# Kernel tuning notes

Measured on AMD Instinct MI355X. Metric: run time of the kernel, lower is better.

Reference implementation:

```python
import jax, jax.numpy as jnp
import numpy as np

B, T, DM = 4, 1024, 1024
H, NW = 16, 16
HD = DM // H  # 64


def _l2norm(x, eps=1e-12):
    n = jnp.sqrt(jnp.sum(x * x, axis=-1, keepdims=True))
    return x / jnp.maximum(n, eps)


def setup_inputs() -> dict:
    key = jax.random.key(0)
    ks = jax.random.split(key, 14)
    s = 0.02
    d = {
        "x": jax.random.normal(ks[0], (B, T, DM), jnp.float32),
        "Wqf": jax.random.normal(ks[1], (H * NW, DM), jnp.float32) * s,
        "bqf": jnp.zeros((H * NW,), jnp.float32),
        "Wkf": jax.random.normal(ks[2], (H * NW, DM), jnp.float32) * s,
        "bkf": jnp.zeros((H * NW,), jnp.float32),
        "Wqp": jax.random.normal(ks[3], (H * NW, DM), jnp.float32) * s,
        "bqp": jnp.zeros((H * NW,), jnp.float32),
        "Wkp": jax.random.normal(ks[4], (H * NW, DM), jnp.float32) * s,
        "bkp": jnp.zeros((H * NW,), jnp.float32),
        "Wv": jax.random.normal(ks[5], (DM, DM), jnp.float32) * s,
        "bv": jnp.zeros((DM,), jnp.float32),
        "Wo": jax.random.normal(ks[6], (DM, DM), jnp.float32) * s,
        "bo": jnp.zeros((DM,), jnp.float32),
        "inter_scale": jnp.ones((H, 1, 1), jnp.float32),
    }
    return d


def reference(x, Wqf, bqf, Wkf, bkf, Wqp, bqp, Wkp, bkp, Wv, bv, Wo, bo, inter_scale):
    b, t, c = x.shape
    # projections -> [b, H, t, NW]
    def proj(W, bb, w_last):
        return (x @ W.T + bb).reshape(b, t, H, w_last).transpose(0, 2, 1, 3)

    q_f = proj(Wqf, bqf, NW)
    k_f = proj(Wkf, bkf, NW)
    q_p = proj(Wqp, bqp, NW)
    k_p = proj(Wkp, bkp, NW)
    v = proj(Wv, bv, HD)  # [b,H,t,HD]

    t_pos = jnp.arange(t, dtype=x.dtype)[None, None, :, None]  # [1,1,t,1]
    q_waves = jnp.sin(q_f * t_pos + q_p)
    k_waves = jnp.sin(k_f * t_pos + k_p)

    scale_factor = NW ** 0.25
    q_norm = _l2norm(q_waves) * scale_factor
    k_norm = _l2norm(k_waves) * scale_factor

    # wave interference scores [b,H,t,t]
    interference = jnp.einsum('bhtw,bhsw->bhts', q_norm, k_norm)
    interference = interference * inter_scale  # broadcast [H,1,1]

    causal = jnp.tril(jnp.ones((t, t), dtype=bool))  # True = attended
    # elu_plus_one kernel; masked positions -> elu(-inf)+1 == 0
    attn = jnp.where(causal, jax.nn.elu(interference) + 1.0, 0.0)

    num_attended = jnp.arange(1, t + 1, dtype=x.dtype)[None, None, :, None]
    attn = attn / jnp.sqrt(num_attended)

    out = jnp.einsum('bhts,bhsd->bhtd', attn, v)  # [b,H,t,HD]
    out = out.transpose(0, 2, 1, 3).reshape(b, t, c)
    return out @ Wo.T + bo
```

## Files before the change

kernel.cpp:

```cpp
#include <hip/hip_runtime.h>
#include <math.h>

typedef __attribute__((ext_vector_type(8))) short bf16x8;
typedef __attribute__((ext_vector_type(4))) float f32x4;
typedef __attribute__((ext_vector_type(4))) int i32x4;

typedef __attribute__((address_space(3))) void lds_void;
typedef __attribute__((address_space(1))) const void glb_cvoid;

__device__ __forceinline__ unsigned short f32_to_bf16(float f) {
    unsigned u = __float_as_uint(f);
    unsigned r = (u + 0x7FFFu + ((u >> 16) & 1u)) >> 16;
    return (unsigned short)r;
}
__device__ __forceinline__ float bf16_to_f32(unsigned short h) {
    return __uint_as_float(((unsigned)h) << 16);
}

__global__ __launch_bounds__(256)
void split_bf16(const float* __restrict__ src, unsigned short* __restrict__ hi,
                unsigned short* __restrict__ lo, int n4)
{
    const int i = blockIdx.x * 256 + threadIdx.x;
    if (i >= n4) return;
    float4 v = *reinterpret_cast<const float4*>(src + (size_t)i * 4);
    ushort4 h;
    h.x = f32_to_bf16(v.x); h.y = f32_to_bf16(v.y);
    h.z = f32_to_bf16(v.z); h.w = f32_to_bf16(v.w);
    *reinterpret_cast<ushort4*>(hi + (size_t)i * 4) = h;
    if (lo) {
        ushort4 l;
        l.x = f32_to_bf16(v.x - bf16_to_f32(h.x));
        l.y = f32_to_bf16(v.y - bf16_to_f32(h.y));
        l.z = f32_to_bf16(v.z - bf16_to_f32(h.z));
        l.w = f32_to_bf16(v.w - bf16_to_f32(h.w));
        *reinterpret_cast<ushort4*>(lo + (size_t)i * 4) = l;
    }
}

__global__ __launch_bounds__(256)
void split4_bf16(const float* __restrict__ W0, const float* __restrict__ W1,
                 const float* __restrict__ W2, const float* __restrict__ W3,
                 unsigned short* __restrict__ hi, unsigned short* __restrict__ lo)
{
    const int i = blockIdx.x * 256 + threadIdx.x;
    const int sel = i >> 16, j = i & 65535;
    const float* W = (sel == 0) ? W0 : (sel == 1) ? W1 : (sel == 2) ? W2 : W3;
    float4 v = *reinterpret_cast<const float4*>(W + (size_t)j * 4);
    ushort4 h, l;
    h.x = f32_to_bf16(v.x); h.y = f32_to_bf16(v.y);
    h.z = f32_to_bf16(v.z); h.w = f32_to_bf16(v.w);
    l.x = f32_to_bf16(v.x - bf16_to_f32(h.x));
    l.y = f32_to_bf16(v.y - bf16_to_f32(h.y));
    l.z = f32_to_bf16(v.z - bf16_to_f32(h.z));
    l.w = f32_to_bf16(v.w - bf16_to_f32(h.w));
    const size_t o = (size_t)sel * 262144 + (size_t)j * 4;
    *reinterpret_cast<ushort4*>(hi + o) = h;
    *reinterpret_cast<ushort4*>(lo + o) = l;
}

template <int MODE>
__global__ __launch_bounds__(256)
void mfma_gemm(const unsigned short* __restrict__ A0,
               const unsigned short* __restrict__ A1,
               const unsigned short* __restrict__ B0,
               const unsigned short* __restrict__ B1,
               const float* __restrict__ bias,
               float* __restrict__ outF, unsigned short* __restrict__ outH)
{
    __shared__ __attribute__((aligned(16))) unsigned short Al[128 * 64];
    __shared__ __attribute__((aligned(16))) unsigned short Bl[64 * 64];

    const int tid = threadIdx.x;
    const int w = tid >> 6, l = tid & 63;
    const int bm = blockIdx.y * 128, bn = blockIdx.x * 64;
    const int KTOT = (MODE == 0) ? 3072 : 1024;
    const int wr = w >> 1, wc = w & 1;
    const int lr = l & 15, lg = l >> 4;
    const int r8 = l >> 3;
    const int c8 = l & 7;
    const int csw = (c8 ^ r8) << 3;

    f32x4 acc[4][2];
#pragma unroll
    for (int i = 0; i < 4; i++)
#pragma unroll
        for (int j = 0; j < 2; j++)
#pragma unroll
            for (int r = 0; r < 4; r++) acc[i][j][r] = 0.f;

    for (int k0 = 0; k0 < KTOT; k0 += 64) {
        const unsigned short* Aseg = A0;
        const unsigned short* Bseg = B0;
        int kc = k0;
        if (MODE == 0) {
            const int seg = k0 >> 10;
            kc = k0 & 1023;
            if (seg == 1) Aseg = A1;
            if (seg == 2) Bseg = B1;
        }
#pragma unroll
        for (int i = 0; i < 4; i++) {
            const int ar = w * 32 + i * 8 + r8;
            __builtin_amdgcn_global_load_lds(
                (glb_cvoid*)(Aseg + (size_t)(bm + ar) * 1024 + kc + csw),
                (lds_void*)(&Al[(w * 32 + i * 8) * 64]), 16, 0, 0);
        }
#pragma unroll
        for (int i = 0; i < 2; i++) {
            const int br = w * 16 + i * 8 + r8;
            __builtin_amdgcn_global_load_lds(
                (glb_cvoid*)(Bseg + (size_t)(bn + br) * 1024 + kc + csw),
                (lds_void*)(&Bl[(w * 16 + i * 8) * 64]), 16, 0, 0);
        }
        __syncthreads();

        bf16x8 af[4][2], bfr[2][2];
#pragma unroll
        for (int i = 0; i < 4; i++)
#pragma unroll
            for (int kk = 0; kk < 2; kk++)
                af[i][kk] = *reinterpret_cast<const bf16x8*>(
                    &Al[(wr * 64 + i * 16 + lr) * 64 +
                        (((kk * 4 + lg) ^ (lr & 7)) << 3)]);
#pragma unroll
        for (int j = 0; j < 2; j++)
#pragma unroll
            for (int kk = 0; kk < 2; kk++)
                bfr[j][kk] = *reinterpret_cast<const bf16x8*>(
                    &Bl[(wc * 32 + j * 16 + lr) * 64 +
                        (((kk * 4 + lg) ^ (lr & 7)) << 3)]);
#pragma unroll
        for (int kk = 0; kk < 2; kk++)
#pragma unroll
            for (int i = 0; i < 4; i++)
#pragma unroll
                for (int j = 0; j < 2; j++)
                    acc[i][j] = __builtin_amdgcn_mfma_f32_16x16x32_bf16(
                        af[i][kk], bfr[j][kk], acc[i][j], 0, 0, 0);
        __syncthreads();
    }

#pragma unroll
    for (int i = 0; i < 4; i++) {
#pragma unroll
        for (int j = 0; j < 2; j++) {
#pragma unroll
            for (int r = 0; r < 4; r++) {
                const int row = bm + wr * 64 + i * 16 + lg * 4 + r;
                const int col = bn + wc * 32 + j * 16 + lr;
                float v = acc[i][j][r];
                if (MODE == 0) {
                    outF[(size_t)row * 1024 + col] = v;
                } else if (MODE == 1) {
                    v += bias[col];
                    const int hh = col >> 6, d = col & 63;
                    const int b = row >> 10, t = row & 1023;
                    outH[(((size_t)(b * 16 + hh) * 64 + d) * 1024) + t] =
                        f32_to_bf16(v);
                } else {
                    outF[(size_t)row * 1024 + col] = v + bias[col];
                }
            }
        }
    }
}

__global__ __launch_bounds__(256)
void wave_norm(const float* __restrict__ raw,
               const float* __restrict__ bqf, const float* __restrict__ bkf,
               const float* __restrict__ bqp, const float* __restrict__ bkp,
               unsigned short* __restrict__ qn, unsigned short* __restrict__ kn)
{
    const int row = blockIdx.x;
    const int b = row >> 10, t = row & 1023;
    const int tid = threadIdx.x;
    const float tf = (float)t;

    const float qf = raw[(size_t)row * 1024 + tid]        + bqf[tid];
    const float kf = raw[(size_t)row * 1024 + 256 + tid]  + bkf[tid];
    const float qp = raw[(size_t)row * 1024 + 512 + tid]  + bqp[tid];
    const float kp = raw[(size_t)row * 1024 + 768 + tid]  + bkp[tid];

    const float sq = sinf(fmaf(qf, tf, qp));
    const float sk = sinf(fmaf(kf, tf, kp));

    float nq = sq * sq, nk = sk * sk;
#pragma unroll
    for (int off = 8; off >= 1; off >>= 1) {
        nq += __shfl_xor(nq, off, 16);
        nk += __shfl_xor(nk, off, 16);
    }
    const float qv = sq * 2.0f / fmaxf(sqrtf(nq), 1e-12f);
    const float kv = sk * 2.0f / fmaxf(sqrtf(nk), 1e-12f);

    const int h = tid >> 4, ww = tid & 15;
    const size_t o = ((size_t)(b * 16 + h) * 1024 + t) * 16 + ww;
    qn[o] = f32_to_bf16(qv);
    kn[o] = f32_to_bf16(kv);
}

__global__ __launch_bounds__(512)
void wave_attn_mfma(const unsigned short* __restrict__ qn,
                    const unsigned short* __restrict__ kn,
                    const unsigned short* __restrict__ vtt,
                    const float* __restrict__ iscale,
                    unsigned short* __restrict__ y)
{
    const int p = blockIdx.x, bh = blockIdx.y;
    const int h = bh & 15, b = bh >> 4;
    const int tid = threadIdx.x;
    const int wq = tid >> 6;
    const int l = tid & 63;
    const int lt = l & 15;
    const int gl = l >> 4;
    const int it = (wq < 4) ? p : (15 - p);
    const int t0w = it * 64 + (wq & 3) * 16;
    const float scale = iscale[h];
    const int tmine = t0w + lt;

    const bf16x8 zero8 = {0, 0, 0, 0, 0, 0, 0, 0};
    const f32x4 zf = {0.f, 0.f, 0.f, 0.f};
    const size_t kb = (size_t)bh * 1024;

    bf16x8 bq = zero8;
    if (gl < 2)
        bq = *reinterpret_cast<const bf16x8*>(&qn[(kb + t0w + lt) * 16 + gl * 8]);

    f32x4 o[4];
#pragma unroll
    for (int jd = 0; jd < 4; jd++) o[jd] = zf;

    const int addr0 = ((2 * (gl & 1)) * 16 + lt) * 4;
    const int addr1 = addr0 + 64;
    const bool hi = ((gl >> 1) & 1) != 0;

    bf16x8 akc[4], akn[4];
#pragma unroll
    for (int js = 0; js < 4; js++) {
        akc[js] = zero8;
        if (gl < 2)
            akc[js] = *reinterpret_cast<const bf16x8*>(
                &kn[(kb + js * 16 + lt) * 16 + gl * 8]);
    }

    for (int is = 0; is <= it; is++) {
        const int s0 = is * 64;

        if (is < it) {
#pragma unroll
            for (int js = 0; js < 4; js++) {
                akn[js] = zero8;
                if (gl < 2)
                    akn[js] = *reinterpret_cast<const bf16x8*>(
                        &kn[(kb + s0 + 64 + js * 16 + lt) * 16 + gl * 8]);
            }
        }
        bf16x8 bv[2][4];
#pragma unroll
        for (int ks = 0; ks < 2; ks++)
#pragma unroll
            for (int jd = 0; jd < 4; jd++)
                bv[ks][jd] = *reinterpret_cast<const bf16x8*>(
                    &vtt[((size_t)(bh * 64 + jd * 16 + lt)) * 1024 +
                         s0 + ks * 32 + gl * 8]);

        f32x4 st[4];
#pragma unroll
        for (int js = 0; js < 4; js++)
            st[js] = __builtin_amdgcn_mfma_f32_16x16x32_bf16(
                akc[js], bq, zf, 0, 0, 0);

        int pk[4][2];
#pragma unroll
        for (int js = 0; js < 4; js++) {
            float pp[4];
#pragma unroll
            for (int r = 0; r < 4; r++) {
                const int s = s0 + js * 16 + gl * 4 + r;
                const float xv = st[js][r] * scale;
                const float phi = (xv > 0.f) ? (xv + 1.0f) : __expf(xv);
                pp[r] = (s <= tmine) ? phi : 0.f;
            }
            asm("v_cvt_pk_bf16_f32 %0, %1, %2"
                : "=v"(pk[js][0]) : "v"(pp[0]), "v"(pp[1]));
            asm("v_cvt_pk_bf16_f32 %0, %1, %2"
                : "=v"(pk[js][1]) : "v"(pp[2]), "v"(pp[3]));
        }

        int rg[4][2][2];
#pragma unroll
        for (int js = 0; js < 4; js++)
#pragma unroll
            for (int sl = 0; sl < 2; sl++) {
                rg[js][sl][0] = __builtin_amdgcn_ds_bpermute(addr0, pk[js][sl]);
                rg[js][sl][1] = __builtin_amdgcn_ds_bpermute(addr1, pk[js][sl]);
            }

#pragma unroll
        for (int ks = 0; ks < 2; ks++) {
            i32x4 au;
#pragma unroll
            for (int c = 0; c < 2; c++)
#pragma unroll
                for (int sl = 0; sl < 2; sl++)
                    au[2 * c + sl] = hi ? rg[2 * ks + 1][sl][c]
                                        : rg[2 * ks][sl][c];
            const bf16x8 pa = __builtin_bit_cast(bf16x8, au);
#pragma unroll
            for (int jd = 0; jd < 4; jd++)
                o[jd] = __builtin_amdgcn_mfma_f32_16x16x32_bf16(
                    pa, bv[ks][jd], o[jd], 0, 0, 0);
        }

#pragma unroll
        for (int js = 0; js < 4; js++) akc[js] = akn[js];
    }

#pragma unroll
    for (int r = 0; r < 4; r++) {
        const int t = t0w + gl * 4 + r;
        const float inv = rsqrtf((float)(t + 1));
#pragma unroll
        for (int jd = 0; jd < 4; jd++) {
            const int d = jd * 16 + lt;
            y[((size_t)b * 1024 + t) * 1024 + h * 64 + d] =
                f32_to_bf16(o[jd][r] * inv);
        }
    }
}

extern "C" void kernel_launch(void* const* d_in, const int* in_sizes, int n_in,
                              void* d_out, int out_size, void* d_ws, size_t ws_size,
                              hipStream_t stream)
{
    const float* x   = (const float*)d_in[0];
    const float* Wqf = (const float*)d_in[1];
    const float* bqf = (const float*)d_in[2];
    const float* Wkf = (const float*)d_in[3];
    const float* bkf = (const float*)d_in[4];
    const float* Wqp = (const float*)d_in[5];
    const float* bqp = (const float*)d_in[6];
    const float* Wkp = (const float*)d_in[7];
    const float* bkp = (const float*)d_in[8];
    const float* Wv  = (const float*)d_in[9];
    const float* bv  = (const float*)d_in[10];
    const float* Wo  = (const float*)d_in[11];
    const float* bo  = (const float*)d_in[12];
    const float* isc = (const float*)d_in[13];
    float* out = (float*)d_out;

    char* ws = (char*)d_ws;
    float*          raw = (float*)(ws);
    unsigned short* ybf = (unsigned short*)(ws);
    unsigned short* xh  = (unsigned short*)(ws + (16u << 20));
    unsigned short* xl  = (unsigned short*)(ws + (24u << 20));
    unsigned short* vtt = (unsigned short*)(ws + (24u << 20));
    unsigned short* WfH = (unsigned short*)(ws + (32u << 20));
    unsigned short* WfL = (unsigned short*)(ws + (34u << 20));
    unsigned short* qn  = (unsigned short*)(ws + (34u << 20));
    unsigned short* kn  = (unsigned short*)(ws + (36u << 20));
    unsigned short* WvH = WfH;
    unsigned short* WoH = WfH;

    split_bf16<<<4096, 256, 0, stream>>>(x, xh, xl, 1048576);
    split4_bf16<<<1024, 256, 0, stream>>>(Wqf, Wkf, Wqp, Wkp, WfH, WfL);

    mfma_gemm<0><<<dim3(16, 32), 256, 0, stream>>>(
        xh, xl, WfH, WfL, nullptr, raw, nullptr);

    split_bf16<<<1024, 256, 0, stream>>>(Wv, WvH, nullptr, 262144);
    mfma_gemm<1><<<dim3(16, 32), 256, 0, stream>>>(
        xh, nullptr, WvH, nullptr, bv, nullptr, vtt);

    wave_norm<<<4096, 256, 0, stream>>>(raw, bqf, bkf, bqp, bkp, qn, kn);

    wave_attn_mfma<<<dim3(8, 64), 512, 0, stream>>>(qn, kn, vtt, isc, ybf);

    split_bf16<<<1024, 256, 0, stream>>>(Wo, WoH, nullptr, 262144);
    mfma_gemm<2><<<dim3(16, 32), 256, 0, stream>>>(
        ybf, nullptr, WoH, nullptr, bo, out, nullptr);
}
```

Baseline: 227.9 us.

## Fuse freq/phase projection GEMM with sine wave normalization epilogue

Replaces the separate 4096x1024 fp32 projection GEMM plus wave_norm pass with one kernel. It computes the frequency GEMM (3-pass bf16 split precision) and the phase GEMM (hi-only bf16) into separate accumulators over the same tile, then applies sin, L2 norm and the bf16 store in the epilogue. This removes the 16MB fp32 raw intermediate write and read and one kernel launch, and drops the lo-split on the phase weights. It also adds an XCD-aware tile remap to all GEMMs. Phase precision drops to single bf16, and the fused GEMM uses smaller 64x64 tiles.

```diff
diff --git a/kernel.cpp b/kernel.cpp
--- a/kernel.cpp
+++ b/kernel.cpp
@@ -39,48 +39,173 @@
 }
 
 __global__ __launch_bounds__(256)
-void split4_bf16(const float* __restrict__ W0, const float* __restrict__ W1,
-                 const float* __restrict__ W2, const float* __restrict__ W3,
-                 unsigned short* __restrict__ hi, unsigned short* __restrict__ lo)
+void split4_bf16(const float* __restrict__ Wqf, const float* __restrict__ Wkf,
+                 const float* __restrict__ Wqp, const float* __restrict__ Wkp,
+                 unsigned short* __restrict__ WfH, unsigned short* __restrict__ WfL,
+                 unsigned short* __restrict__ WpH)
 {
     const int i = blockIdx.x * 256 + threadIdx.x;
     const int sel = i >> 16, j = i & 65535;
-    const float* W = (sel == 0) ? W0 : (sel == 1) ? W1 : (sel == 2) ? W2 : W3;
+    const float* W = (sel == 0) ? Wqf : (sel == 1) ? Wkf : (sel == 2) ? Wqp : Wkp;
     float4 v = *reinterpret_cast<const float4*>(W + (size_t)j * 4);
-    ushort4 h, l;
+    ushort4 h;
     h.x = f32_to_bf16(v.x); h.y = f32_to_bf16(v.y);
     h.z = f32_to_bf16(v.z); h.w = f32_to_bf16(v.w);
-    l.x = f32_to_bf16(v.x - bf16_to_f32(h.x));
-    l.y = f32_to_bf16(v.y - bf16_to_f32(h.y));
-    l.z = f32_to_bf16(v.z - bf16_to_f32(h.z));
-    l.w = f32_to_bf16(v.w - bf16_to_f32(h.w));
-    const size_t o = (size_t)sel * 262144 + (size_t)j * 4;
-    *reinterpret_cast<ushort4*>(hi + o) = h;
-    *reinterpret_cast<ushort4*>(lo + o) = l;
-}
-
-template <int MODE>
+    const size_t o = (size_t)(sel & 1) * 262144 + (size_t)j * 4;
+    if (sel < 2) {
+        *reinterpret_cast<ushort4*>(WfH + o) = h;
+        ushort4 l;
+        l.x = f32_to_bf16(v.x - bf16_to_f32(h.x));
+        l.y = f32_to_bf16(v.y - bf16_to_f32(h.y));
+        l.z = f32_to_bf16(v.z - bf16_to_f32(h.z));
+        l.w = f32_to_bf16(v.w - bf16_to_f32(h.w));
+        *reinterpret_cast<ushort4*>(WfL + o) = l;
+    } else {
+        *reinterpret_cast<ushort4*>(WpH + o) = h;
+    }
+}
+
+__device__ __forceinline__ void xcd_tiles(int& tm, int& tn) {
+    const int L = blockIdx.x + gridDim.x * blockIdx.y;
+    const int nbn = gridDim.x;
+    const int q3 = L >> 3;
+    tn = q3 % nbn;
+    tm = (L & 7) + 8 * (q3 / nbn);
+}
+
 __global__ __launch_bounds__(256)
-void mfma_gemm(const unsigned short* __restrict__ A0,
-               const unsigned short* __restrict__ A1,
-               const unsigned short* __restrict__ B0,
-               const unsigned short* __restrict__ B1,
-               const float* __restrict__ bias,
-               float* __restrict__ outF, unsigned short* __restrict__ outH)
-{
-    __shared__ __attribute__((aligned(16))) unsigned short Al[128 * 64];
+void freq_gemm_norm(const unsigned short* __restrict__ xh,
+                    const unsigned short* __restrict__ xl,
+                    const unsigned short* __restrict__ WfH,
+                    const unsigned short* __restrict__ WfL,
+                    const unsigned short* __restrict__ WpH,
+                    const float* __restrict__ bqf, const float* __restrict__ bkf,
+                    const float* __restrict__ bqp, const float* __restrict__ bkp,
+                    unsigned short* __restrict__ qn, unsigned short* __restrict__ kn)
+{
+    __shared__ __attribute__((aligned(16))) unsigned short Al[64 * 64];
     __shared__ __attribute__((aligned(16))) unsigned short Bl[64 * 64];
+
+    int tm, tn;
+    xcd_tiles(tm, tn);
+    const int bm = tm * 64, bn = tn * 64;
 
     const int tid = threadIdx.x;
     const int w = tid >> 6, l = tid & 63;
-    const int bm = blockIdx.y * 128, bn = blockIdx.x * 64;
-    const int KTOT = (MODE == 0) ? 3072 : 1024;
     const int wr = w >> 1, wc = w & 1;
     const int lr = l & 15, lg = l >> 4;
     const int r8 = l >> 3;
     const int c8 = l & 7;
     const int csw = (c8 ^ r8) << 3;
 
+    f32x4 accF[2][2], accP[2][2];
+#pragma unroll
+    for (int i = 0; i < 2; i++)
+#pragma unroll
+        for (int j = 0; j < 2; j++)
+#pragma unroll
+            for (int r = 0; r < 4; r++) { accF[i][j][r] = 0.f; accP[i][j][r] = 0.f; }
+
+    for (int k0 = 0; k0 < 4096; k0 += 64) {
+        const int seg = k0 >> 10;
+        const int kc = k0 & 1023;
+        const unsigned short* Aseg = (seg == 1) ? xl : xh;
+        const unsigned short* Bseg = (seg <= 1) ? WfH : (seg == 2) ? WfL : WpH;
+
+#pragma unroll
+        for (int i = 0; i < 2; i++) {
+            __builtin_amdgcn_global_load_lds(
+                (glb_cvoid*)(Aseg + (size_t)(bm + w * 16 + i * 8 + r8) * 1024 + kc + csw),
+                (lds_void*)(&Al[(w * 16 + i * 8) * 64]), 16, 0, 0);
+            __builtin_amdgcn_global_load_lds(
+                (glb_cvoid*)(Bseg + (size_t)(bn + w * 16 + i * 8 + r8) * 1024 + kc + csw),
+                (lds_void*)(&Bl[(w * 16 + i * 8) * 64]), 16, 0, 0);
+        }
+        __syncthreads();
+
+        bf16x8 af[2][2], bfr[2][2];
+#pragma unroll
+        for (int i = 0; i < 2; i++)
+#pragma unroll
+            for (int kk = 0; kk < 2; kk++) {
+                af[i][kk] = *reinterpret_cast<const bf16x8*>(
+                    &Al[(wr * 32 + i * 16 + lr) * 64 + (((kk * 4 + lg) ^ (lr & 7)) << 3)]);
+                bfr[i][kk] = *reinterpret_cast<const bf16x8*>(
+                    &Bl[(wc * 32 + i * 16 + lr) * 64 + (((kk * 4 + lg) ^ (lr & 7)) << 3)]);
+            }
+        if (seg < 3) {
+#pragma unroll
+            for (int kk = 0; kk < 2; kk++)
+#pragma unroll
+                for (int i = 0; i < 2; i++)
+#pragma unroll
+                    for (int j = 0; j < 2; j++)
+                        accF[i][j] = __builtin_amdgcn_mfma_f32_16x16x32_bf16(
+                            af[i][kk], bfr[j][kk], accF[i][j], 0, 0, 0);
+        } else {
+#pragma unroll
+            for (int kk = 0; kk < 2; kk++)
+#pragma unroll
+                for (int i = 0; i < 2; i++)
+#pragma unroll
+                    for (int j = 0; j < 2; j++)
+                        accP[i][j] = __builtin_amdgcn_mfma_f32_16x16x32_bf16(
+                            af[i][kk], bfr[j][kk], accP[i][j], 0, 0, 0);
+        }
+        __syncthreads();
+    }
+
+#pragma unroll
+    for (int i = 0; i < 2; i++) {
+#pragma unroll
+        for (int j = 0; j < 2; j++) {
+            const int col = bn + wc * 32 + j * 16 + lr;
+            const bool isQ = col < 256;
+            const int c = col & 255;
+            const float bf = isQ ? bqf[c] : bkf[c];
+            const float bp = isQ ? bqp[c] : bkp[c];
+            unsigned short* dst = isQ ? qn : kn;
+            const int h = c >> 4, ww = c & 15;
+#pragma unroll
+            for (int r = 0; r < 4; r++) {
+                const int row = bm + wr * 32 + i * 16 + lg * 4 + r;
+                const int b = row >> 10, t = row & 1023;
+                const float f = accF[i][j][r] + bf;
+                const float p = accP[i][j][r] + bp;
+                const float s = sinf(fmaf(f, (float)t, p));
+                float n2 = s * s;
+#pragma unroll
+                for (int off = 8; off >= 1; off >>= 1)
+                    n2 += __shfl_xor(n2, off);
+                const float val = s * 2.0f / fmaxf(sqrtf(n2), 1e-12f);
+                dst[((size_t)(b * 16 + h) * 1024 + t) * 16 + ww] = f32_to_bf16(val);
+            }
+        }
+    }
+}
+
+template <int MODE>
+__global__ __launch_bounds__(256)
+void mfma_gemm(const unsigned short* __restrict__ A0,
+               const unsigned short* __restrict__ B0,
+               const float* __restrict__ bias,
+               float* __restrict__ outF, unsigned short* __restrict__ outH)
+{
+    __shared__ __attribute__((aligned(16))) unsigned short Al[128 * 64];
+    __shared__ __attribute__((aligned(16))) unsigned short Bl[64 * 64];
+
+    int tm, tn;
+    xcd_tiles(tm, tn);
+    const int bm = tm * 128, bn = tn * 64;
+
+    const int tid = threadIdx.x;
+    const int w = tid >> 6, l = tid & 63;
+    const int wr = w >> 1, wc = w & 1;
+    const int lr = l & 15, lg = l >> 4;
+    const int r8 = l >> 3;
+    const int c8 = l & 7;
+    const int csw = (c8 ^ r8) << 3;
+
     f32x4 acc[4][2];
 #pragma unroll
     for (int i = 0; i < 4; i++)
@@ -89,28 +214,17 @@
 #pragma unroll
             for (int r = 0; r < 4; r++) acc[i][j][r] = 0.f;
 
-    for (int k0 = 0; k0 < KTOT; k0 += 64) {
-        const unsigned short* Aseg = A0;
-        const unsigned short* Bseg = B0;
-        int kc = k0;
-        if (MODE == 0) {
-            const int seg = k0 >> 10;
-            kc = k0 & 1023;
-            if (seg == 1) Aseg = A1;
-            if (seg == 2) Bseg = B1;
-        }
+    for (int k0 = 0; k0 < 1024; k0 += 64) {
 #pragma unroll
         for (int i = 0; i < 4; i++) {
-            const int ar = w * 32 + i * 8 + r8;
             __builtin_amdgcn_global_load_lds(
-                (glb_cvoid*)(Aseg + (size_t)(bm + ar) * 1024 + kc + csw),
+                (glb_cvoid*)(A0 + (size_t)(bm + w * 32 + i * 8 + r8) * 1024 + k0 + csw),
                 (lds_void*)(&Al[(w * 32 + i * 8) * 64]), 16, 0, 0);
         }
 #pragma unroll
         for (int i = 0; i < 2; i++) {
-            const int br = w * 16 + i * 8 + r8;
             __builtin_amdgcn_global_load_lds(
-                (glb_cvoid*)(Bseg + (size_t)(bn + br) * 1024 + kc + csw),
+                (glb_cvoid*)(B0 + (size_t)(bn + w * 16 + i * 8 + r8) * 1024 + k0 + csw),
                 (lds_void*)(&Bl[(w * 16 + i * 8) * 64]), 16, 0, 0);
         }
         __syncthreads();
@@ -121,15 +235,13 @@
 #pragma unroll
             for (int kk = 0; kk < 2; kk++)
                 af[i][kk] = *reinterpret_cast<const bf16x8*>(
-                    &Al[(wr * 64 + i * 16 + lr) * 64 +
-                        (((kk * 4 + lg) ^ (lr & 7)) << 3)]);
+                    &Al[(wr * 64 + i * 16 + lr) * 64 + (((kk * 4 + lg) ^ (lr & 7)) << 3)]);
 #pragma unroll
         for (int j = 0; j < 2; j++)
 #pragma unroll
             for (int kk = 0; kk < 2; kk++)
                 bfr[j][kk] = *reinterpret_cast<const bf16x8*>(
-                    &Bl[(wc * 32 + j * 16 + lr) * 64 +
-                        (((kk * 4 + lg) ^ (lr & 7)) << 3)]);
+                    &Bl[(wc * 32 + j * 16 + lr) * 64 + (((kk * 4 + lg) ^ (lr & 7)) << 3)]);
 #pragma unroll
         for (int kk = 0; kk < 2; kk++)
 #pragma unroll
@@ -149,55 +261,18 @@
             for (int r = 0; r < 4; r++) {
                 const int row = bm + wr * 64 + i * 16 + lg * 4 + r;
                 const int col = bn + wc * 32 + j * 16 + lr;
-                float v = acc[i][j][r];
-                if (MODE == 0) {
-                    outF[(size_t)row * 1024 + col] = v;
-                } else if (MODE == 1) {
-                    v += bias[col];
+                float v = acc[i][j][r] + bias[col];
+                if (MODE == 1) {
                     const int hh = col >> 6, d = col & 63;
                     const int b = row >> 10, t = row & 1023;
                     outH[(((size_t)(b * 16 + hh) * 64 + d) * 1024) + t] =
                         f32_to_bf16(v);
                 } else {
-                    outF[(size_t)row * 1024 + col] = v + bias[col];
+                    outF[(size_t)row * 1024 + col] = v;
                 }
             }
         }
     }
-}
-
-__global__ __launch_bounds__(256)
-void wave_norm(const float* __restrict__ raw,
-               const float* __restrict__ bqf, const float* __restrict__ bkf,
-               const float* __restrict__ bqp, const float* __restrict__ bkp,
-               unsigned short* __restrict__ qn, unsigned short* __restrict__ kn)
-{
-    const int row = blockIdx.x;
-    const int b = row >> 10, t = row & 1023;
-    const int tid = threadIdx.x;
-    const float tf = (float)t;
-
-    const float qf = raw[(size_t)row * 1024 + tid]        + bqf[tid];
-    const float kf = raw[(size_t)row * 1024 + 256 + tid]  + bkf[tid];
-    const float qp = raw[(size_t)row * 1024 + 512 + tid]  + bqp[tid];
-    const float kp = raw[(size_t)row * 1024 + 768 + tid]  + bkp[tid];
-
-    const float sq = sinf(fmaf(qf, tf, qp));
-    const float sk = sinf(fmaf(kf, tf, kp));
-
-    float nq = sq * sq, nk = sk * sk;
-#pragma unroll
-    for (int off = 8; off >= 1; off >>= 1) {
-        nq += __shfl_xor(nq, off, 16);
-        nk += __shfl_xor(nk, off, 16);
-    }
-    const float qv = sq * 2.0f / fmaxf(sqrtf(nq), 1e-12f);
-    const float kv = sk * 2.0f / fmaxf(sqrtf(nk), 1e-12f);
-
-    const int h = tid >> 4, ww = tid & 15;
-    const size_t o = ((size_t)(b * 16 + h) * 1024 + t) * 16 + ww;
-    qn[o] = f32_to_bf16(qv);
-    kn[o] = f32_to_bf16(kv);
 }
 
 __global__ __launch_bounds__(512)
@@ -351,33 +426,29 @@
     float* out = (float*)d_out;
 
     char* ws = (char*)d_ws;
-    float*          raw = (float*)(ws);
     unsigned short* ybf = (unsigned short*)(ws);
+    unsigned short* qn  = (unsigned short*)(ws + ( 8u << 20));
+    unsigned short* kn  = (unsigned short*)(ws + (10u << 20));
+    unsigned short* WfH = (unsigned short*)(ws + (12u << 20));
+    unsigned short* WfL = (unsigned short*)(ws + (13u << 20));
+    unsigned short* WpH = (unsigned short*)(ws + (14u << 20));
     unsigned short* xh  = (unsigned short*)(ws + (16u << 20));
     unsigned short* xl  = (unsigned short*)(ws + (24u << 20));
     unsigned short* vtt = (unsigned short*)(ws + (24u << 20));
-    unsigned short* WfH = (unsigned short*)(ws + (32u << 20));
-    unsigned short* WfL = (unsigned short*)(ws + (34u << 20));
-    unsigned short* qn  = (unsigned short*)(ws + (34u << 20));
-    unsigned short* kn  = (unsigned short*)(ws + (36u << 20));
-    unsigned short* WvH = WfH;
-    unsigned short* WoH = WfH;
+    unsigned short* WvH = (unsigned short*)(ws + (32u << 20));
+    unsigned short* WoH = WvH;
 
     split_bf16<<<4096, 256, 0, stream>>>(x, xh, xl, 1048576);
-    split4_bf16<<<1024, 256, 0, stream>>>(Wqf, Wkf, Wqp, Wkp, WfH, WfL);
-
-    mfma_gemm<0><<<dim3(16, 32), 256, 0, stream>>>(
-        xh, xl, WfH, WfL, nullptr, raw, nullptr);
+    split4_bf16<<<1024, 256, 0, stream>>>(Wqf, Wkf, Wqp, Wkp, WfH, WfL, WpH);
+
+    freq_gemm_norm<<<dim3(8, 64), 256, 0, stream>>>(
+        xh, xl, WfH, WfL, WpH, bqf, bkf, bqp, bkp, qn, kn);
 
     split_bf16<<<1024, 256, 0, stream>>>(Wv, WvH, nullptr, 262144);
-    mfma_gemm<1><<<dim3(16, 32), 256, 0, stream>>>(
-        xh, nullptr, WvH, nullptr, bv, nullptr, vtt);
-
-    wave_norm<<<4096, 256, 0, stream>>>(raw, bqf, bkf, bqp, bkp, qn, kn);
+    mfma_gemm<1><<<dim3(16, 32), 256, 0, stream>>>(xh, WvH, bv, nullptr, vtt);
 
     wave_attn_mfma<<<dim3(8, 64), 512, 0, stream>>>(qn, kn, vtt, isc, ybf);
 
     split_bf16<<<1024, 256, 0, stream>>>(Wo, WoH, nullptr, 262144);
-    mfma_gemm<2><<<dim3(16, 32), 256, 0, stream>>>(
-        ybf, nullptr, WoH, nullptr, bo, out, nullptr);
-}
+    mfma_gemm<2><<<dim3(16, 32), 256, 0, stream>>>(ybf, WoH, bo, out, nullptr);
+}
```

After: 227.2 us. No clear change (-0.3%).
